# Performance work log

Hardware: AMD Instinct MI355X
Metric: run time of the kernel (lower is better)

The kernel has to match this reference:

```python
import jax, jax.numpy as jnp
import numpy as np

B, N, C, H = 8, 1024, 768, 12
D = C // H          # head_dim = 64
M = 2 * D           # rand_feat_dim = 128
SCALE = D ** -0.5
EPS = 1e-12         # F.normalize eps


def _feature_map(z, rand_matrix):
    # z: [B,H,N,D] already multiplied by sqrt(scale); proj: [H,D,M]
    logits = jnp.einsum('bhnd,hdm->bhnm', z, rand_matrix)
    sqnorm = 0.5 * jnp.sum(z * z, axis=-1, keepdims=True)
    return jnp.exp(logits - sqnorm) * (M ** -0.5)


def setup_inputs() -> dict:
    key = jax.random.key(0)
    k1, k2, k3, k4, k5 = jax.random.split(key, 5)
    x = jax.random.normal(k1, (B, N, C), dtype=jnp.float32)
    qkv_w = jax.random.normal(k2, (3 * C, C), dtype=jnp.float32) * 0.02
    proj_w = jax.random.normal(k3, (C, C), dtype=jnp.float32) * 0.02
    proj_b = jax.random.normal(k4, (C,), dtype=jnp.float32) * 0.02
    rand_matrix = jax.random.normal(k5, (H, D, M), dtype=jnp.float32)
    return {"x": x, "qkv_w": qkv_w, "proj_w": proj_w, "proj_b": proj_b,
            "rand_matrix": rand_matrix}


def reference(x, qkv_w, proj_w, proj_b, rand_matrix):
    b, n, c = x.shape
    # qkv projection (torch Linear, no bias): [B,N,3C] -> [3,B,H,N,D]
    qkv = (x @ qkv_w.T).reshape(b, n, 3, H, D).transpose(2, 0, 3, 1, 4)
    q, k, v = qkv[0], qkv[1], qkv[2]
    sq = SCALE ** 0.5
    qf = _feature_map(q * sq, rand_matrix)   # [B,H,N,M]
    kf = _feature_map(k * sq, rand_matrix)   # [B,H,N,M]
    attn = jnp.einsum('bhnm,bhkm->bhnk', qf, kf)          # explicit O(N^2)
    denom = jnp.maximum(jnp.sum(jnp.abs(attn), axis=-1, keepdims=True), EPS)
    attn = attn / denom                                   # L1 normalize
    out = jnp.einsum('bhnk,bhkd->bhnd', attn, v)          # [B,H,N,D]
    out = out.transpose(0, 2, 1, 3).reshape(b, n, c)
    return out @ proj_w.T + proj_b
```

## Files before the change

kernel.cpp:

```cpp
#include <hip/hip_runtime.h>
#include <hip/hip_bf16.h>

#define PB 8
#define PN 1024
#define PC 768
#define PH 12
#define PD 64
#define PM 128
#define SQ 0.35355339059327373f
#define MSCALE 0.08838834764831843f

typedef _Float16 f16;
typedef f16 f16x8 __attribute__((ext_vector_type(8)));
typedef f16 f16x4 __attribute__((ext_vector_type(4)));
typedef float f32x4 __attribute__((ext_vector_type(4)));

#define GLL(src, dst) __builtin_amdgcn_global_load_lds( \
    (const __attribute__((address_space(1))) void*)(src), \
    (__attribute__((address_space(3))) void*)(dst), 16, 0, 0)

__global__ __launch_bounds__(192) void conv_all(
        const float* __restrict__ x, const float* __restrict__ qkv_w,
        const float* __restrict__ proj_w, const float* __restrict__ rm,
        f16* __restrict__ Ax, f16* __restrict__ Bqk, f16* __restrict__ Bp,
        f16* __restrict__ Rt, float* __restrict__ kvf, float* __restrict__ sf)
{
    const int bid = blockIdx.x;
    const int t = threadIdx.x;
    if (bid < 11264) {
        const float* src; f16* dst; int r;
        if (bid < 8192)       { src = x;      dst = Ax;  r = bid; }
        else if (bid < 10496) { src = qkv_w;  dst = Bqk; r = bid - 8192; }
        else                  { src = proj_w; dst = Bp;  r = bid - 10496; }
        const int c = t * 4;
        float4 v = *(const float4*)&src[(size_t)r * PC + c];
        f16x4 hv;
        hv.x = (f16)v.x; hv.y = (f16)v.y; hv.z = (f16)v.z; hv.w = (f16)v.w;
        *(f16x4*)&dst[(size_t)r * PC + c] = hv;
    } else if (bid < 11276) {
        const int h = bid - 11264;
        for (int e = t; e < PD * PM; e += 192)
            Rt[(size_t)h * 8192 + e] = (f16)rm[(size_t)h * 8192 + (e & 63) * PM + (e >> 6)];
    } else if (bid < 12300) {
        float4 z = make_float4(0.f, 0.f, 0.f, 0.f);
        *(float4*)&kvf[(size_t)(bid - 11276) * 768 + t * 4] = z;
    } else {
        float4 z = make_float4(0.f, 0.f, 0.f, 0.f);
        *(float4*)&sf[(size_t)(bid - 12300) * 768 + t * 4] = z;
    }
}

__global__ __launch_bounds__(256) void gemm_qkv(
        const f16* __restrict__ A,
        const f16* __restrict__ Bm,
        f16* __restrict__ zq, f16* __restrict__ zk, f16* __restrict__ vh,
        float* __restrict__ sqq, float* __restrict__ sqk)
{
    __shared__ f16 As[128 * 64];
    __shared__ f16 Bs[128 * 64];
    const int t = threadIdx.x;
    const int wave = t >> 6, lane = t & 63;
    const int wm = wave >> 1, wn = wave & 1;
    const int bi = blockIdx.x * 128, bj = blockIdx.y * 128;

    f32x4 acc[4][4] = {};

    const int rowi = lane >> 3;
    const int cb = (lane & 7) ^ ((lane >> 4) & 3);
    const f16* ApE = A + (size_t)(bi + wave * 32 + rowi) * PC + cb * 8;
    const f16* ApO = A + (size_t)(bi + wave * 32 + rowi) * PC + (cb ^ 4) * 8;
    const f16* BpE = Bm + (size_t)(bj + wave * 32 + rowi) * PC + cb * 8;
    const f16* BpO = Bm + (size_t)(bj + wave * 32 + rowi) * PC + (cb ^ 4) * 8;
    f16* AsB = &As[wave * 32 * 64];
    f16* BsB = &Bs[wave * 32 * 64];

    const int q4 = lane >> 4;
    for (int kt = 0; kt < 12; ++kt) {
        const int k0 = kt * 64;
        __syncthreads();
        GLL(ApE + k0,               AsB);
        GLL(ApO + k0 + (size_t) 8 * PC, AsB + 8 * 64);
        GLL(ApE + k0 + (size_t)16 * PC, AsB + 16 * 64);
        GLL(ApO + k0 + (size_t)24 * PC, AsB + 24 * 64);
        GLL(BpE + k0,               BsB);
        GLL(BpO + k0 + (size_t) 8 * PC, BsB + 8 * 64);
        GLL(BpE + k0 + (size_t)16 * PC, BsB + 16 * 64);
        GLL(BpO + k0 + (size_t)24 * PC, BsB + 24 * 64);
        __syncthreads();

        #pragma unroll
        for (int kh = 0; kh < 2; ++kh) {
            f16x8 af[4], bf[4];
            #pragma unroll
            for (int i = 0; i < 4; ++i) {
                const int r = wm * 64 + i * 16 + (lane & 15);
                const int p = (kh * 4 + q4) ^ ((r >> 1) & 7);
                af[i] = *(const f16x8*)&As[r * 64 + p * 8];
            }
            #pragma unroll
            for (int j = 0; j < 4; ++j) {
                const int r = wn * 64 + j * 16 + (lane & 15);
                const int p = (kh * 4 + q4) ^ ((r >> 1) & 7);
                bf[j] = *(const f16x8*)&Bs[r * 64 + p * 8];
            }
            #pragma unroll
            for (int i = 0; i < 4; ++i)
                #pragma unroll
                for (int j = 0; j < 4; ++j)
                    acc[i][j] = __builtin_amdgcn_mfma_f32_16x16x32_f16(af[i], bf[j], acc[i][j], 0, 0, 0);
        }
    }

    const int quad = lane >> 4, cc = lane & 15;
    const int colbase = bj + wn * 64;
    const int b = bi >> 10;
    if (colbase < 1536) {
        const int which = colbase >= 768;
        const int h = (colbase - which * 768) >> 6;
        f16* zdst = which ? zk : zq;
        float* sdst = which ? sqk : sqq;
        const size_t bh = (size_t)(b * PH + h);
        #pragma unroll
        for (int i = 0; i < 4; ++i) {
            const int row0 = bi + wm * 64 + i * 16 + quad * 4;
            #pragma unroll
            for (int r = 0; r < 4; ++r) {
                const int n = (row0 + r) & 1023;
                f16 zh[4]; float psq = 0.f;
                #pragma unroll
                for (int j = 0; j < 4; ++j) {
                    zh[j] = (f16)(acc[i][j][r] * SQ);
                    float zf = (float)zh[j];
                    psq += zf * zf;
                }
                psq += __shfl_xor(psq, 1, 64);
                psq += __shfl_xor(psq, 2, 64);
                psq += __shfl_xor(psq, 4, 64);
                psq += __shfl_xor(psq, 8, 64);
                if (cc == 0) sdst[(bh << 10) + n] = 0.5f * psq;
                f16* zp = zdst + (((bh << 10) + n) << 6);
                #pragma unroll
                for (int j = 0; j < 4; ++j) zp[j * 16 + cc] = zh[j];
            }
        }
    } else {
        const int h = (colbase - 1536) >> 6;
        const size_t bh = (size_t)(b * PH + h);
        #pragma unroll
        for (int i = 0; i < 4; ++i) {
            const int row0 = bi + wm * 64 + i * 16 + quad * 4;
            #pragma unroll
            for (int r = 0; r < 4; ++r) {
                const int n = (row0 + r) & 1023;
                f16* vp = vh + (((bh << 10) + n) << 6);
                #pragma unroll
                for (int j = 0; j < 4; ++j) vp[j * 16 + cc] = (f16)acc[i][j][r];
            }
        }
    }
}

__global__ __launch_bounds__(256) void feat_kv(
        const f16* __restrict__ zk, const f16* __restrict__ Rt,
        const float* __restrict__ sqk, const f16* __restrict__ vh,
        float* __restrict__ kvf, float* __restrict__ sf)
{
    __shared__ __align__(16) char smem[52224];
    f16* As = (f16*)smem;
    f16* Bs = (f16*)(smem + 16384);
    f16* Pt = (f16*)smem;
    f16* vT = (f16*)(smem + 34816);
    __shared__ float sqs[128];

    const int t = threadIdx.x;
    const int wave = t >> 6, lane = t & 63;
    const int wm = wave >> 1, wn = wave & 1;
    const int nt = blockIdx.x, bh = blockIdx.y;
    const int h = bh % PH;

    const f16* A = zk + (((size_t)bh << 10) + nt * 128) * 64;
    const f16* Bm = Rt + (size_t)h * (PM * PD);

    if (t < 128) sqs[t] = sqk[((size_t)bh << 10) + nt * 128 + t];

    const int rowi = lane >> 3;
    const int cb = (lane & 7) ^ ((lane >> 4) & 3);
    const f16* ApE = A + (size_t)(wave * 32 + rowi) * 64 + cb * 8;
    const f16* ApO = A + (size_t)(wave * 32 + rowi) * 64 + (cb ^ 4) * 8;
    const f16* BpE = Bm + (size_t)(wave * 32 + rowi) * 64 + cb * 8;
    const f16* BpO = Bm + (size_t)(wave * 32 + rowi) * 64 + (cb ^ 4) * 8;
    f16* AsB = &As[wave * 32 * 64];
    f16* BsB = &Bs[wave * 32 * 64];
    GLL(ApE,            AsB);
    GLL(ApO + 8 * 64,   AsB + 8 * 64);
    GLL(ApE + 16 * 64,  AsB + 16 * 64);
    GLL(ApO + 24 * 64,  AsB + 24 * 64);
    GLL(BpE,            BsB);
    GLL(BpO + 8 * 64,   BsB + 8 * 64);
    GLL(BpE + 16 * 64,  BsB + 16 * 64);
    GLL(BpO + 24 * 64,  BsB + 24 * 64);
    __syncthreads();

    const int q4 = lane >> 4;
    f32x4 acc[4][4] = {};
    #pragma unroll
    for (int kh = 0; kh < 2; ++kh) {
        f16x8 af[4], bf[4];
        #pragma unroll
        for (int i = 0; i < 4; ++i) {
            const int r = wm * 64 + i * 16 + (lane & 15);
            const int p = (kh * 4 + q4) ^ ((r >> 1) & 7);
            af[i] = *(const f16x8*)&As[r * 64 + p * 8];
        }
        #pragma unroll
        for (int j = 0; j < 4; ++j) {
            const int r = wn * 64 + j * 16 + (lane & 15);
            const int p = (kh * 4 + q4) ^ ((r >> 1) & 7);
            bf[j] = *(const f16x8*)&Bs[r * 64 + p * 8];
        }
        #pragma unroll
        for (int i = 0; i < 4; ++i)
            #pragma unroll
            for (int j = 0; j < 4; ++j)
                acc[i][j] = __builtin_amdgcn_mfma_f32_16x16x32_f16(af[i], bf[j], acc[i][j], 0, 0, 0);
    }

    const int quad = lane >> 4, cc = lane & 15;
    __syncthreads();

    #pragma unroll
    for (int i = 0; i < 4; ++i) {
        #pragma unroll
        for (int j = 0; j < 4; ++j) {
            const int col = wn * 64 + j * 16 + cc;
            #pragma unroll
            for (int r = 0; r < 4; ++r) {
                const int rl = wm * 64 + i * 16 + quad * 4 + r;
                Pt[col * 136 + rl] = (f16)(__expf(acc[i][j][r] - sqs[rl]) * MSCALE);
            }
        }
    }
    {
        const int vn = t >> 1;
        const int vhf = (t & 1) * 32;
        const f16* vbase = vh + (((size_t)bh << 10) + nt * 128 + vn) * 64 + vhf;
        #pragma unroll
        for (int k = 0; k < 4; ++k) {
            f16x8 vv = *(const f16x8*)&vbase[k * 8];
            #pragma unroll
            for (int e = 0; e < 8; ++e)
                vT[(vhf + k * 8 + e) * 136 + vn] = vv[e];
        }
    }
    __syncthreads();

    f32x4 acc2[4][2] = {};
    #pragma unroll
    for (int kt = 0; kt < 4; ++kt) {
        const int kb = kt * 32 + (lane >> 4) * 8;
        f16x8 af2[4], bf2[2];
        #pragma unroll
        for (int i = 0; i < 4; ++i)
            af2[i] = *(const f16x8*)&Pt[(wm * 64 + i * 16 + (lane & 15)) * 136 + kb];
        #pragma unroll
        for (int j = 0; j < 2; ++j)
            bf2[j] = *(const f16x8*)&vT[(wn * 32 + j * 16 + (lane & 15)) * 136 + kb];
        #pragma unroll
        for (int i = 0; i < 4; ++i)
            #pragma unroll
            for (int j = 0; j < 2; ++j)
                acc2[i][j] = __builtin_amdgcn_mfma_f32_16x16x32_f16(af2[i], bf2[j], acc2[i][j], 0, 0, 0);
    }

    float* kvo = kvf + (size_t)bh * 8192;
    #pragma unroll
    for (int i = 0; i < 4; ++i) {
        #pragma unroll
        for (int j = 0; j < 2; ++j) {
            const int d = wn * 32 + j * 16 + cc;
            #pragma unroll
            for (int r = 0; r < 4; ++r) {
                const int m = wm * 64 + i * 16 + quad * 4 + r;
                atomicAdd(&kvo[m * 64 + d], acc2[i][j][r]);
            }
        }
    }
    {
        const int sm = t >> 1, shf = (t & 1) * 64;
        float sp = 0.f;
        #pragma unroll
        for (int k = 0; k < 8; ++k) {
            f16x8 pv = *(const f16x8*)&Pt[sm * 136 + shf + k * 8];
            #pragma unroll
            for (int e = 0; e < 8; ++e) sp += (float)pv[e];
        }
        sp += __shfl_xor(sp, 1, 64);
        if ((t & 1) == 0) atomicAdd(&sf[(size_t)bh * 128 + sm], sp);
    }
}

__global__ __launch_bounds__(256) void feat_apply(
        const f16* __restrict__ zq, const f16* __restrict__ Rt,
        const float* __restrict__ sqq, const float* __restrict__ kvf,
        const float* __restrict__ sf, f16* __restrict__ ohA)
{
    __shared__ __align__(16) char smem[52224];
    f16* As = (f16*)smem;
    f16* Bs = (f16*)(smem + 16384);
    f16* Pn = (f16*)smem;
    f16* kvT = (f16*)(smem + 34816);
    __shared__ float sqs[128], ssm[128], dns[128];

    const int t = threadIdx.x;
    const int wave = t >> 6, lane = t & 63;
    const int wm = wave >> 1, wn = wave & 1;
    const int nt = blockIdx.x, bh = blockIdx.y;
    const int b = bh / PH, h = bh % PH;

    const f16* A = zq + (((size_t)bh << 10) + nt * 128) * 64;
    const f16* Bm = Rt + (size_t)h * (PM * PD);

    if (t < 128) {
        sqs[t] = sqq[((size_t)bh << 10) + nt * 128 + t];
        ssm[t] = sf[(size_t)bh * 128 + t];
    }

    const int rowi = lane >> 3;
    const int cb = (lane & 7) ^ ((lane >> 4) & 3);
    const f16* ApE = A + (size_t)(wave * 32 + rowi) * 64 + cb * 8;
    const f16* ApO = A + (size_t)(wave * 32 + rowi) * 64 + (cb ^ 4) * 8;
    const f16* BpE = Bm + (size_t)(wave * 32 + rowi) * 64 + cb * 8;
    const f16* BpO = Bm + (size_t)(wave * 32 + rowi) * 64 + (cb ^ 4) * 8;
    f16* AsB = &As[wave * 32 * 64];
    f16* BsB = &Bs[wave * 32 * 64];
    GLL(ApE,            AsB);
    GLL(ApO + 8 * 64,   AsB + 8 * 64);
    GLL(ApE + 16 * 64,  AsB + 16 * 64);
    GLL(ApO + 24 * 64,  AsB + 24 * 64);
    GLL(BpE,            BsB);
    GLL(BpO + 8 * 64,   BsB + 8 * 64);
    GLL(BpE + 16 * 64,  BsB + 16 * 64);
    GLL(BpO + 24 * 64,  BsB + 24 * 64);
    __syncthreads();

    const int q4 = lane >> 4;
    f32x4 acc[4][4] = {};
    #pragma unroll
    for (int kh = 0; kh < 2; ++kh) {
        f16x8 af[4], bf[4];
        #pragma unroll
        for (int i = 0; i < 4; ++i) {
            const int r = wm * 64 + i * 16 + (lane & 15);
            const int p = (kh * 4 + q4) ^ ((r >> 1) & 7);
            af[i] = *(const f16x8*)&As[r * 64 + p * 8];
        }
        #pragma unroll
        for (int j = 0; j < 4; ++j) {
            const int r = wn * 64 + j * 16 + (lane & 15);
            const int p = (kh * 4 + q4) ^ ((r >> 1) & 7);
            bf[j] = *(const f16x8*)&Bs[r * 64 + p * 8];
        }
        #pragma unroll
        for (int i = 0; i < 4; ++i)
            #pragma unroll
            for (int j = 0; j < 4; ++j)
                acc[i][j] = __builtin_amdgcn_mfma_f32_16x16x32_f16(af[i], bf[j], acc[i][j], 0, 0, 0);
    }

    const int quad = lane >> 4, cc = lane & 15;
    __syncthreads();

    #pragma unroll
    for (int i = 0; i < 4; ++i) {
        #pragma unroll
        for (int j = 0; j < 4; ++j) {
            const int col = wn * 64 + j * 16 + cc;
            #pragma unroll
            for (int r = 0; r < 4; ++r) {
                const int rl = wm * 64 + i * 16 + quad * 4 + r;
                Pn[rl * 136 + col] = (f16)(__expf(acc[i][j][r] - sqs[rl]) * MSCALE);
            }
        }
    }
    {
        const int m = t >> 1;
        const int dh2 = (t & 1) * 32;
        const float* kvb = kvf + ((size_t)bh * 128 + m) * 64 + dh2;
        #pragma unroll
        for (int k = 0; k < 8; ++k) {
            float4 k4 = *(const float4*)&kvb[k * 4];
            kvT[(dh2 + k * 4 + 0) * 136 + m] = (f16)k4.x;
            kvT[(dh2 + k * 4 + 1) * 136 + m] = (f16)k4.y;
            kvT[(dh2 + k * 4 + 2) * 136 + m] = (f16)k4.z;
            kvT[(dh2 + k * 4 + 3) * 136 + m] = (f16)k4.w;
        }
    }
    __syncthreads();

    {
        const int n = t >> 1, mh = (t & 1) * 64;
        float p = 0.f;
        #pragma unroll
        for (int k = 0; k < 8; ++k) {
            f16x8 pv = *(const f16x8*)&Pn[n * 136 + mh + k * 8];
            #pragma unroll
            for (int e = 0; e < 8; ++e)
                p += (float)pv[e] * ssm[mh + k * 8 + e];
        }
        p += __shfl_xor(p, 1, 64);
        if ((t & 1) == 0) dns[n] = (p < 1e-12f) ? 1e-12f : p;
    }
    __syncthreads();

    f32x4 acc3[4][2] = {};
    #pragma unroll
    for (int kt = 0; kt < 4; ++kt) {
        const int kb = kt * 32 + (lane >> 4) * 8;
        f16x8 af3[4], bf3[2];
        #pragma unroll
        for (int i = 0; i < 4; ++i)
            af3[i] = *(const f16x8*)&Pn[(wm * 64 + i * 16 + (lane & 15)) * 136 + kb];
        #pragma unroll
        for (int j = 0; j < 2; ++j)
            bf3[j] = *(const f16x8*)&kvT[(wn * 32 + j * 16 + (lane & 15)) * 136 + kb];
        #pragma unroll
        for (int i = 0; i < 4; ++i)
            #pragma unroll
            for (int j = 0; j < 2; ++j)
                acc3[i][j] = __builtin_amdgcn_mfma_f32_16x16x32_f16(af3[i], bf3[j], acc3[i][j], 0, 0, 0);
    }

    f16* ob = ohA + ((size_t)(b * PN) + nt * 128) * PC + h * PD;
    #pragma unroll
    for (int i = 0; i < 4; ++i) {
        #pragma unroll
        for (int j = 0; j < 2; ++j) {
            const int d = wn * 32 + j * 16 + cc;
            #pragma unroll
            for (int r = 0; r < 4; ++r) {
                const int n = wm * 64 + i * 16 + quad * 4 + r;
                ob[(size_t)n * PC + d] = (f16)(acc3[i][j][r] / dns[n]);
            }
        }
    }
}

__global__ __launch_bounds__(256) void gemm_proj(
        const f16* __restrict__ A,
        const f16* __restrict__ Bm,
        float* __restrict__ Cm, const float* __restrict__ bias)
{
    __shared__ f16 As[128 * 64];
    __shared__ f16 Bs[64 * 64];
    const int t = threadIdx.x;
    const int wave = t >> 6, lane = t & 63;
    const int wm = wave >> 1, wn = wave & 1;
    const int bi = blockIdx.x * 128, bj = blockIdx.y * 64;

    f32x4 acc[4][2] = {};

    const int rowi = lane >> 3;
    const int cb = (lane & 7) ^ ((lane >> 4) & 3);
    const f16* ApE = A + (size_t)(bi + wave * 32 + rowi) * PC + cb * 8;
    const f16* ApO = A + (size_t)(bi + wave * 32 + rowi) * PC + (cb ^ 4) * 8;
    const f16* BpE = Bm + (size_t)(bj + wave * 16 + rowi) * PC + cb * 8;
    const f16* BpO = Bm + (size_t)(bj + wave * 16 + rowi) * PC + (cb ^ 4) * 8;
    f16* AsB = &As[wave * 32 * 64];
    f16* BsB = &Bs[wave * 16 * 64];

    const int q4 = lane >> 4;
    for (int kt = 0; kt < 12; ++kt) {
        const int k0 = kt * 64;
        __syncthreads();
        GLL(ApE + k0,               AsB);
        GLL(ApO + k0 + (size_t) 8 * PC, AsB + 8 * 64);
        GLL(ApE + k0 + (size_t)16 * PC, AsB + 16 * 64);
        GLL(ApO + k0 + (size_t)24 * PC, AsB + 24 * 64);
        GLL(BpE + k0,               BsB);
        GLL(BpO + k0 + (size_t) 8 * PC, BsB + 8 * 64);
        __syncthreads();

        #pragma unroll
        for (int kh = 0; kh < 2; ++kh) {
            f16x8 af[4], bf[2];
            #pragma unroll
            for (int i = 0; i < 4; ++i) {
                const int r = wm * 64 + i * 16 + (lane & 15);
                const int p = (kh * 4 + q4) ^ ((r >> 1) & 7);
                af[i] = *(const f16x8*)&As[r * 64 + p * 8];
            }
            #pragma unroll
            for (int j = 0; j < 2; ++j) {
                const int r = wn * 32 + j * 16 + (lane & 15);
                const int p = (kh * 4 + q4) ^ ((r >> 1) & 7);
                bf[j] = *(const f16x8*)&Bs[r * 64 + p * 8];
            }
            #pragma unroll
            for (int i = 0; i < 4; ++i)
                #pragma unroll
                for (int j = 0; j < 2; ++j)
                    acc[i][j] = __builtin_amdgcn_mfma_f32_16x16x32_f16(af[i], bf[j], acc[i][j], 0, 0, 0);
        }
    }

    const int cr = (lane >> 4) * 4, cc = lane & 15;
    #pragma unroll
    for (int i = 0; i < 4; ++i) {
        const int row = bi + wm * 64 + i * 16 + cr;
        #pragma unroll
        for (int j = 0; j < 2; ++j) {
            const int col = bj + wn * 32 + j * 16 + cc;
            const float bv = bias[col];
            #pragma unroll
            for (int r = 0; r < 4; ++r)
                Cm[(size_t)(row + r) * PC + col] = acc[i][j][r] + bv;
        }
    }
}

extern "C" void kernel_launch(void* const* d_in, const int* in_sizes, int n_in,
                              void* d_out, int out_size, void* d_ws, size_t ws_size,
                              hipStream_t stream) {
    const float* x      = (const float*)d_in[0];
    const float* qkv_w  = (const float*)d_in[1];
    const float* proj_w = (const float*)d_in[2];
    const float* proj_b = (const float*)d_in[3];
    const float* rm     = (const float*)d_in[4];
    float* out = (float*)d_out;

    char* ws = (char*)d_ws;
    f16*   Ax   = (f16*)(ws);
    f16*   Bqk  = (f16*)(ws + 12582912);
    f16*   Bp   = (f16*)(ws + 16121856);
    f16*   Rt   = (f16*)(ws + 17301504);
    f16*   zq   = (f16*)(ws + 17498112);
    f16*   zk   = (f16*)(ws + 30081024);
    f16*   vh   = (f16*)(ws + 42663936);
    float* sqq  = (float*)(ws + 55246848);
    float* sqk  = (float*)(ws + 55640064);
    float* kvf  = (float*)(ws + 56033280);
    float* sf   = (float*)(ws + 59179008);
    f16*   ohA  = (f16*)(ws + 59228160);

    conv_all<<<12316, 192, 0, stream>>>(x, qkv_w, proj_w, rm, Ax, Bqk, Bp, Rt, kvf, sf);

    gemm_qkv<<<dim3(64, 18), 256, 0, stream>>>(Ax, Bqk, zq, zk, vh, sqq, sqk);

    feat_kv<<<dim3(8, 96), 256, 0, stream>>>(zk, Rt, sqk, vh, kvf, sf);

    feat_apply<<<dim3(8, 96), 256, 0, stream>>>(zq, Rt, sqq, kvf, sf, ohA);

    gemm_proj<<<dim3(64, 12), 256, 0, stream>>>(ohA, Bp, out, proj_b);
}
```

Baseline: 191.1 us.

## Double-buffer GEMM LDS tiles and replace KV atomics with partial-sum reduction

Both GEMM kernels now stage the next K tile into a second LDS buffer while computing on the current one, hiding global-load latency at the cost of doubled shared memory. feat_kv writes per-tile partial KV and feature sums to workspace buffers instead of using atomicAdd, and a new kv_reduce kernel sums them. This also removes the zero-init blocks from the conversion kernel. V and KV loads are hoisted earlier to overlap with the first GEMM stage, and the partial buffers reuse dead workspace regions.

```diff
diff --git a/kernel.cpp b/kernel.cpp
--- a/kernel.cpp
+++ b/kernel.cpp
@@ -23,7 +23,7 @@
         const float* __restrict__ x, const float* __restrict__ qkv_w,
         const float* __restrict__ proj_w, const float* __restrict__ rm,
         f16* __restrict__ Ax, f16* __restrict__ Bqk, f16* __restrict__ Bp,
-        f16* __restrict__ Rt, float* __restrict__ kvf, float* __restrict__ sf)
+        f16* __restrict__ Rt)
 {
     const int bid = blockIdx.x;
     const int t = threadIdx.x;
@@ -37,16 +37,10 @@
         f16x4 hv;
         hv.x = (f16)v.x; hv.y = (f16)v.y; hv.z = (f16)v.z; hv.w = (f16)v.w;
         *(f16x4*)&dst[(size_t)r * PC + c] = hv;
-    } else if (bid < 11276) {
+    } else {
         const int h = bid - 11264;
         for (int e = t; e < PD * PM; e += 192)
             Rt[(size_t)h * 8192 + e] = (f16)rm[(size_t)h * 8192 + (e & 63) * PM + (e >> 6)];
-    } else if (bid < 12300) {
-        float4 z = make_float4(0.f, 0.f, 0.f, 0.f);
-        *(float4*)&kvf[(size_t)(bid - 11276) * 768 + t * 4] = z;
-    } else {
-        float4 z = make_float4(0.f, 0.f, 0.f, 0.f);
-        *(float4*)&sf[(size_t)(bid - 12300) * 768 + t * 4] = z;
     }
 }
 
@@ -56,8 +50,8 @@
         f16* __restrict__ zq, f16* __restrict__ zk, f16* __restrict__ vh,
         float* __restrict__ sqq, float* __restrict__ sqk)
 {
-    __shared__ f16 As[128 * 64];
-    __shared__ f16 Bs[128 * 64];
+    __shared__ f16 As[2][8192];
+    __shared__ f16 Bs[2][8192];
     const int t = threadIdx.x;
     const int wave = t >> 6, lane = t & 63;
     const int wm = wave >> 1, wn = wave & 1;
@@ -71,22 +65,24 @@
     const f16* ApO = A + (size_t)(bi + wave * 32 + rowi) * PC + (cb ^ 4) * 8;
     const f16* BpE = Bm + (size_t)(bj + wave * 32 + rowi) * PC + cb * 8;
     const f16* BpO = Bm + (size_t)(bj + wave * 32 + rowi) * PC + (cb ^ 4) * 8;
-    f16* AsB = &As[wave * 32 * 64];
-    f16* BsB = &Bs[wave * 32 * 64];
+
+#define STG(BUF, KT) do { const int k0_ = (KT) * 64; \
+    GLL(ApE + k0_,                   &As[BUF][wave * 2048]); \
+    GLL(ApO + k0_ + (size_t) 8 * PC, &As[BUF][wave * 2048 +  512]); \
+    GLL(ApE + k0_ + (size_t)16 * PC, &As[BUF][wave * 2048 + 1024]); \
+    GLL(ApO + k0_ + (size_t)24 * PC, &As[BUF][wave * 2048 + 1536]); \
+    GLL(BpE + k0_,                   &Bs[BUF][wave * 2048]); \
+    GLL(BpO + k0_ + (size_t) 8 * PC, &Bs[BUF][wave * 2048 +  512]); \
+    GLL(BpE + k0_ + (size_t)16 * PC, &Bs[BUF][wave * 2048 + 1024]); \
+    GLL(BpO + k0_ + (size_t)24 * PC, &Bs[BUF][wave * 2048 + 1536]); } while(0)
 
     const int q4 = lane >> 4;
+    STG(0, 0);
+    __syncthreads();
+
     for (int kt = 0; kt < 12; ++kt) {
-        const int k0 = kt * 64;
-        __syncthreads();
-        GLL(ApE + k0,               AsB);
-        GLL(ApO + k0 + (size_t) 8 * PC, AsB + 8 * 64);
-        GLL(ApE + k0 + (size_t)16 * PC, AsB + 16 * 64);
-        GLL(ApO + k0 + (size_t)24 * PC, AsB + 24 * 64);
-        GLL(BpE + k0,               BsB);
-        GLL(BpO + k0 + (size_t) 8 * PC, BsB + 8 * 64);
-        GLL(BpE + k0 + (size_t)16 * PC, BsB + 16 * 64);
-        GLL(BpO + k0 + (size_t)24 * PC, BsB + 24 * 64);
-        __syncthreads();
+        const int cur = kt & 1;
+        if (kt < 11) STG(cur ^ 1, kt + 1);
 
         #pragma unroll
         for (int kh = 0; kh < 2; ++kh) {
@@ -95,13 +91,13 @@
             for (int i = 0; i < 4; ++i) {
                 const int r = wm * 64 + i * 16 + (lane & 15);
                 const int p = (kh * 4 + q4) ^ ((r >> 1) & 7);
-                af[i] = *(const f16x8*)&As[r * 64 + p * 8];
+                af[i] = *(const f16x8*)&As[cur][r * 64 + p * 8];
             }
             #pragma unroll
             for (int j = 0; j < 4; ++j) {
                 const int r = wn * 64 + j * 16 + (lane & 15);
                 const int p = (kh * 4 + q4) ^ ((r >> 1) & 7);
-                bf[j] = *(const f16x8*)&Bs[r * 64 + p * 8];
+                bf[j] = *(const f16x8*)&Bs[cur][r * 64 + p * 8];
             }
             #pragma unroll
             for (int i = 0; i < 4; ++i)
@@ -109,7 +105,9 @@
                 for (int j = 0; j < 4; ++j)
                     acc[i][j] = __builtin_amdgcn_mfma_f32_16x16x32_f16(af[i], bf[j], acc[i][j], 0, 0, 0);
         }
-    }
+        __syncthreads();
+    }
+#undef STG
 
     const int quad = lane >> 4, cc = lane & 15;
     const int colbase = bj + wn * 64;
@@ -163,7 +161,7 @@
 __global__ __launch_bounds__(256) void feat_kv(
         const f16* __restrict__ zk, const f16* __restrict__ Rt,
         const float* __restrict__ sqk, const f16* __restrict__ vh,
-        float* __restrict__ kvf, float* __restrict__ sf)
+        float* __restrict__ kvpA, float* __restrict__ kvpB, float* __restrict__ sfp)
 {
     __shared__ __align__(16) char smem[52224];
     f16* As = (f16*)smem;
@@ -182,6 +180,14 @@
     const f16* Bm = Rt + (size_t)h * (PM * PD);
 
     if (t < 128) sqs[t] = sqk[((size_t)bh << 10) + nt * 128 + t];
+
+    const int vn = t >> 1;
+    const int vhf = (t & 1) * 32;
+    const f16* vbase = vh + (((size_t)bh << 10) + nt * 128 + vn) * 64 + vhf;
+    f16x8 vpre0 = *(const f16x8*)&vbase[0];
+    f16x8 vpre1 = *(const f16x8*)&vbase[8];
+    f16x8 vpre2 = *(const f16x8*)&vbase[16];
+    f16x8 vpre3 = *(const f16x8*)&vbase[24];
 
     const int rowi = lane >> 3;
     const int cb = (lane & 7) ^ ((lane >> 4) & 3);
@@ -241,15 +247,12 @@
         }
     }
     {
-        const int vn = t >> 1;
-        const int vhf = (t & 1) * 32;
-        const f16* vbase = vh + (((size_t)bh << 10) + nt * 128 + vn) * 64 + vhf;
-        #pragma unroll
-        for (int k = 0; k < 4; ++k) {
-            f16x8 vv = *(const f16x8*)&vbase[k * 8];
-            #pragma unroll
-            for (int e = 0; e < 8; ++e)
-                vT[(vhf + k * 8 + e) * 136 + vn] = vv[e];
+        #pragma unroll
+        for (int e = 0; e < 8; ++e) {
+            vT[(vhf +      e) * 136 + vn] = vpre0[e];
+            vT[(vhf +  8 + e) * 136 + vn] = vpre1[e];
+            vT[(vhf + 16 + e) * 136 + vn] = vpre2[e];
+            vT[(vhf + 24 + e) * 136 + vn] = vpre3[e];
         }
     }
     __syncthreads();
@@ -272,7 +275,8 @@
                 acc2[i][j] = __builtin_amdgcn_mfma_f32_16x16x32_f16(af2[i], bf2[j], acc2[i][j], 0, 0, 0);
     }
 
-    float* kvo = kvf + (size_t)bh * 8192;
+    float* kvo = ((nt < 4) ? (kvpA + (size_t)nt * 786432)
+                           : (kvpB + (size_t)(nt - 4) * 786432)) + (size_t)bh * 8192;
     #pragma unroll
     for (int i = 0; i < 4; ++i) {
         #pragma unroll
@@ -281,7 +285,7 @@
             #pragma unroll
             for (int r = 0; r < 4; ++r) {
                 const int m = wm * 64 + i * 16 + quad * 4 + r;
-                atomicAdd(&kvo[m * 64 + d], acc2[i][j][r]);
+                kvo[m * 64 + d] = acc2[i][j][r];
             }
         }
     }
@@ -295,8 +299,39 @@
             for (int e = 0; e < 8; ++e) sp += (float)pv[e];
         }
         sp += __shfl_xor(sp, 1, 64);
-        if ((t & 1) == 0) atomicAdd(&sf[(size_t)bh * 128 + sm], sp);
-    }
+        if ((t & 1) == 0) sfp[((size_t)nt * 96 + bh) * 128 + sm] = sp;
+    }
+}
+
+__global__ __launch_bounds__(256) void kv_reduce(
+        const float* __restrict__ kvpA, const float* __restrict__ kvpB,
+        const float* __restrict__ sfp, float* __restrict__ kvf, float* __restrict__ sf)
+{
+    const int bh = blockIdx.x;
+    if (blockIdx.y == 8) {
+        const int t = threadIdx.x;
+        if (t < 128) {
+            float s = 0.f;
+            #pragma unroll
+            for (int nt = 0; nt < 8; ++nt)
+                s += sfp[((size_t)nt * 96 + bh) * 128 + t];
+            sf[(size_t)bh * 128 + t] = s;
+        }
+        return;
+    }
+    const size_t base = (size_t)bh * 8192 + blockIdx.y * 1024 + threadIdx.x * 4;
+    float4 s = *(const float4*)&kvpA[base];
+    #pragma unroll
+    for (int nt = 1; nt < 4; ++nt) {
+        float4 v = *(const float4*)&kvpA[(size_t)nt * 786432 + base];
+        s.x += v.x; s.y += v.y; s.z += v.z; s.w += v.w;
+    }
+    #pragma unroll
+    for (int nt = 0; nt < 4; ++nt) {
+        float4 v = *(const float4*)&kvpB[(size_t)nt * 786432 + base];
+        s.x += v.x; s.y += v.y; s.z += v.z; s.w += v.w;
+    }
+    *(float4*)&kvf[base] = s;
 }
 
 __global__ __launch_bounds__(256) void feat_apply(
@@ -324,6 +359,13 @@
         sqs[t] = sqq[((size_t)bh << 10) + nt * 128 + t];
         ssm[t] = sf[(size_t)bh * 128 + t];
     }
+
+    const int m_ = t >> 1;
+    const int dh2 = (t & 1) * 32;
+    const float* kvb = kvf + ((size_t)bh * 128 + m_) * 64 + dh2;
+    float4 kpre[8];
+    #pragma unroll
+    for (int k = 0; k < 8; ++k) kpre[k] = *(const float4*)&kvb[k * 4];
 
     const int rowi = lane >> 3;
     const int cb = (lane & 7) ^ ((lane >> 4) & 3);
@@ -383,16 +425,12 @@
         }
     }
     {
-        const int m = t >> 1;
-        const int dh2 = (t & 1) * 32;
-        const float* kvb = kvf + ((size_t)bh * 128 + m) * 64 + dh2;
         #pragma unroll
         for (int k = 0; k < 8; ++k) {
-            float4 k4 = *(const float4*)&kvb[k * 4];
-            kvT[(dh2 + k * 4 + 0) * 136 + m] = (f16)k4.x;
-            kvT[(dh2 + k * 4 + 1) * 136 + m] = (f16)k4.y;
-            kvT[(dh2 + k * 4 + 2) * 136 + m] = (f16)k4.z;
-            kvT[(dh2 + k * 4 + 3) * 136 + m] = (f16)k4.w;
+            kvT[(dh2 + k * 4 + 0) * 136 + m_] = (f16)kpre[k].x;
+            kvT[(dh2 + k * 4 + 1) * 136 + m_] = (f16)kpre[k].y;
+            kvT[(dh2 + k * 4 + 2) * 136 + m_] = (f16)kpre[k].z;
+            kvT[(dh2 + k * 4 + 3) * 136 + m_] = (f16)kpre[k].w;
         }
     }
     __syncthreads();
@@ -450,8 +488,8 @@
         const f16* __restrict__ Bm,
         float* __restrict__ Cm, const float* __restrict__ bias)
 {
-    __shared__ f16 As[128 * 64];
-    __shared__ f16 Bs[64 * 64];
+    __shared__ f16 As[2][8192];
+    __shared__ f16 Bs[2][4096];
     const int t = threadIdx.x;
     const int wave = t >> 6, lane = t & 63;
     const int wm = wave >> 1, wn = wave & 1;
@@ -465,20 +503,22 @@
     const f16* ApO = A + (size_t)(bi + wave * 32 + rowi) * PC + (cb ^ 4) * 8;
     const f16* BpE = Bm + (size_t)(bj + wave * 16 + rowi) * PC + cb * 8;
     const f16* BpO = Bm + (size_t)(bj + wave * 16 + rowi) * PC + (cb ^ 4) * 8;
-    f16* AsB = &As[wave * 32 * 64];
-    f16* BsB = &Bs[wave * 16 * 64];
+
+#define STGP(BUF, KT) do { const int k0_ = (KT) * 64; \
+    GLL(ApE + k0_,                   &As[BUF][wave * 2048]); \
+    GLL(ApO + k0_ + (size_t) 8 * PC, &As[BUF][wave * 2048 +  512]); \
+    GLL(ApE + k0_ + (size_t)16 * PC, &As[BUF][wave * 2048 + 1024]); \
+    GLL(ApO + k0_ + (size_t)24 * PC, &As[BUF][wave * 2048 + 1536]); \
+    GLL(BpE + k0_,                   &Bs[BUF][wave * 1024]); \
+    GLL(BpO + k0_ + (size_t) 8 * PC, &Bs[BUF][wave * 1024 + 512]); } while(0)
 
     const int q4 = lane >> 4;
+    STGP(0, 0);
+    __syncthreads();
+
     for (int kt = 0; kt < 12; ++kt) {
-        const int k0 = kt * 64;
-        __syncthreads();
-        GLL(ApE + k0,               AsB);
-        GLL(ApO + k0 + (size_t) 8 * PC, AsB + 8 * 64);
-        GLL(ApE + k0 + (size_t)16 * PC, AsB + 16 * 64);
-        GLL(ApO + k0 + (size_t)24 * PC, AsB + 24 * 64);
-        GLL(BpE + k0,               BsB);
-        GLL(BpO + k0 + (size_t) 8 * PC, BsB + 8 * 64);
-        __syncthreads();
+        const int cur = kt & 1;
+        if (kt < 11) STGP(cur ^ 1, kt + 1);
 
         #pragma unroll
         for (int kh = 0; kh < 2; ++kh) {
@@ -487,13 +527,13 @@
             for (int i = 0; i < 4; ++i) {
                 const int r = wm * 64 + i * 16 + (lane & 15);
                 const int p = (kh * 4 + q4) ^ ((r >> 1) & 7);
-                af[i] = *(const f16x8*)&As[r * 64 + p * 8];
+                af[i] = *(const f16x8*)&As[cur][r * 64 + p * 8];
             }
             #pragma unroll
             for (int j = 0; j < 2; ++j) {
                 const int r = wn * 32 + j * 16 + (lane & 15);
                 const int p = (kh * 4 + q4) ^ ((r >> 1) & 7);
-                bf[j] = *(const f16x8*)&Bs[r * 64 + p * 8];
+                bf[j] = *(const f16x8*)&Bs[cur][r * 64 + p * 8];
             }
             #pragma unroll
             for (int i = 0; i < 4; ++i)
@@ -501,7 +541,9 @@
                 for (int j = 0; j < 2; ++j)
                     acc[i][j] = __builtin_amdgcn_mfma_f32_16x16x32_f16(af[i], bf[j], acc[i][j], 0, 0, 0);
         }
-    }
+        __syncthreads();
+    }
+#undef STGP
 
     const int cr = (lane >> 4) * 4, cc = lane & 15;
     #pragma unroll
@@ -542,11 +584,17 @@
     float* sf   = (float*)(ws + 59179008);
     f16*   ohA  = (f16*)(ws + 59228160);
 
-    conv_all<<<12316, 192, 0, stream>>>(x, qkv_w, proj_w, rm, Ax, Bqk, Bp, Rt, kvf, sf);
+    float* kvpA = (float*)(ws);
+    float* kvpB = (float*)(ws + 59228160);
+    float* sfp  = (float*)(ws + 12582912);
+
+    conv_all<<<11276, 192, 0, stream>>>(x, qkv_w, proj_w, rm, Ax, Bqk, Bp, Rt);
 
     gemm_qkv<<<dim3(64, 18), 256, 0, stream>>>(Ax, Bqk, zq, zk, vh, sqq, sqk);
 
-    feat_kv<<<dim3(8, 96), 256, 0, stream>>>(zk, Rt, sqk, vh, kvf, sf);
+    feat_kv<<<dim3(8, 96), 256, 0, stream>>>(zk, Rt, sqk, vh, kvpA, kvpB, sfp);
+
+    kv_reduce<<<dim3(96, 9), 256, 0, stream>>>(kvpA, kvpB, sfp, kvf, sf);
 
     feat_apply<<<dim3(8, 96), 256, 0, stream>>>(zq, Rt, sqq, kvf, sf, ohA);
 
```

Result: no change. 193.0 us (+1.0%).

## Stage QKV epilogue through LDS and replace KV atomics with partial-sum reduction

Applied to the files above, without the earlier changes.

The QKV GEMM epilogue now writes each wave's 64x64 tile into swizzled shared memory. It then stores it to zq/zk/vh as coalesced 16-byte row segments, instead of scattered 2-byte stores. feat_kv no longer does float atomicAdd into kvf and sf. It writes per-tile partial results into scratch buffers that alias dead workspace regions, and a new kv_reduce kernel sums the eight partials. This removes the atomic traffic and the zero-initialisation blocks in conv_all, at the cost of an extra kernel launch and roughly 25 MB of extra partial-buffer reads and writes.

```diff
diff --git a/kernel.cpp b/kernel.cpp
--- a/kernel.cpp
+++ b/kernel.cpp
@@ -23,7 +23,7 @@
         const float* __restrict__ x, const float* __restrict__ qkv_w,
         const float* __restrict__ proj_w, const float* __restrict__ rm,
         f16* __restrict__ Ax, f16* __restrict__ Bqk, f16* __restrict__ Bp,
-        f16* __restrict__ Rt, float* __restrict__ kvf, float* __restrict__ sf)
+        f16* __restrict__ Rt)
 {
     const int bid = blockIdx.x;
     const int t = threadIdx.x;
@@ -37,16 +37,10 @@
         f16x4 hv;
         hv.x = (f16)v.x; hv.y = (f16)v.y; hv.z = (f16)v.z; hv.w = (f16)v.w;
         *(f16x4*)&dst[(size_t)r * PC + c] = hv;
-    } else if (bid < 11276) {
+    } else {
         const int h = bid - 11264;
         for (int e = t; e < PD * PM; e += 192)
             Rt[(size_t)h * 8192 + e] = (f16)rm[(size_t)h * 8192 + (e & 63) * PM + (e >> 6)];
-    } else if (bid < 12300) {
-        float4 z = make_float4(0.f, 0.f, 0.f, 0.f);
-        *(float4*)&kvf[(size_t)(bid - 11276) * 768 + t * 4] = z;
-    } else {
-        float4 z = make_float4(0.f, 0.f, 0.f, 0.f);
-        *(float4*)&sf[(size_t)(bid - 12300) * 768 + t * 4] = z;
     }
 }
 
@@ -111,9 +105,14 @@
         }
     }
 
+    __syncthreads();
+    f16* W = (wave < 2 ? As : Bs) + (wave & 1) * 4096;
     const int quad = lane >> 4, cc = lane & 15;
+    const int rr = lane >> 3, c8 = lane & 7;
     const int colbase = bj + wn * 64;
     const int b = bi >> 10;
+    const int nb = (bi & 1023) + wm * 64;
+
     if (colbase < 1536) {
         const int which = colbase >= 768;
         const int h = (colbase - which * 768) >> 6;
@@ -122,10 +121,9 @@
         const size_t bh = (size_t)(b * PH + h);
         #pragma unroll
         for (int i = 0; i < 4; ++i) {
-            const int row0 = bi + wm * 64 + i * 16 + quad * 4;
             #pragma unroll
             for (int r = 0; r < 4; ++r) {
-                const int n = (row0 + r) & 1023;
+                const int li = i * 16 + quad * 4 + r;
                 f16 zh[4]; float psq = 0.f;
                 #pragma unroll
                 for (int j = 0; j < 4; ++j) {
@@ -137,25 +135,40 @@
                 psq += __shfl_xor(psq, 2, 64);
                 psq += __shfl_xor(psq, 4, 64);
                 psq += __shfl_xor(psq, 8, 64);
-                if (cc == 0) sdst[(bh << 10) + n] = 0.5f * psq;
-                f16* zp = zdst + (((bh << 10) + n) << 6);
+                if (cc == 0) sdst[(bh << 10) + nb + li] = 0.5f * psq;
                 #pragma unroll
-                for (int j = 0; j < 4; ++j) zp[j * 16 + cc] = zh[j];
-            }
+                for (int j = 0; j < 4; ++j)
+                    W[li * 64 + ((j * 16 + cc) ^ (quad << 4))] = zh[j];
+            }
+        }
+        asm volatile("" ::: "memory");
+        #pragma unroll
+        for (int it = 0; it < 8; ++it) {
+            const int row = it * 8 + rr;
+            const int s = ((row >> 2) & 3) << 4;
+            f16x8 vv = *(const f16x8*)&W[row * 64 + ((c8 * 8) ^ s)];
+            *(f16x8*)&zdst[(((bh << 10) + nb + row) << 6) + c8 * 8] = vv;
         }
     } else {
         const int h = (colbase - 1536) >> 6;
         const size_t bh = (size_t)(b * PH + h);
         #pragma unroll
         for (int i = 0; i < 4; ++i) {
-            const int row0 = bi + wm * 64 + i * 16 + quad * 4;
             #pragma unroll
             for (int r = 0; r < 4; ++r) {
-                const int n = (row0 + r) & 1023;
-                f16* vp = vh + (((bh << 10) + n) << 6);
+                const int li = i * 16 + quad * 4 + r;
                 #pragma unroll
-                for (int j = 0; j < 4; ++j) vp[j * 16 + cc] = (f16)acc[i][j][r];
-            }
+                for (int j = 0; j < 4; ++j)
+                    W[li * 64 + ((j * 16 + cc) ^ (quad << 4))] = (f16)acc[i][j][r];
+            }
+        }
+        asm volatile("" ::: "memory");
+        #pragma unroll
+        for (int it = 0; it < 8; ++it) {
+            const int row = it * 8 + rr;
+            const int s = ((row >> 2) & 3) << 4;
+            f16x8 vv = *(const f16x8*)&W[row * 64 + ((c8 * 8) ^ s)];
+            *(f16x8*)&vh[(((bh << 10) + nb + row) << 6) + c8 * 8] = vv;
         }
     }
 }
@@ -163,7 +176,7 @@
 __global__ __launch_bounds__(256) void feat_kv(
         const f16* __restrict__ zk, const f16* __restrict__ Rt,
         const float* __restrict__ sqk, const f16* __restrict__ vh,
-        float* __restrict__ kvf, float* __restrict__ sf)
+        float* __restrict__ kvpA, float* __restrict__ kvpB, float* __restrict__ sfp)
 {
     __shared__ __align__(16) char smem[52224];
     f16* As = (f16*)smem;
@@ -272,7 +285,8 @@
                 acc2[i][j] = __builtin_amdgcn_mfma_f32_16x16x32_f16(af2[i], bf2[j], acc2[i][j], 0, 0, 0);
     }
 
-    float* kvo = kvf + (size_t)bh * 8192;
+    float* kvo = ((nt < 4) ? (kvpA + (size_t)nt * 786432)
+                           : (kvpB + (size_t)(nt - 4) * 786432)) + (size_t)bh * 8192;
     #pragma unroll
     for (int i = 0; i < 4; ++i) {
         #pragma unroll
@@ -281,7 +295,7 @@
             #pragma unroll
             for (int r = 0; r < 4; ++r) {
                 const int m = wm * 64 + i * 16 + quad * 4 + r;
-                atomicAdd(&kvo[m * 64 + d], acc2[i][j][r]);
+                kvo[m * 64 + d] = acc2[i][j][r];
             }
         }
     }
@@ -295,8 +309,39 @@
             for (int e = 0; e < 8; ++e) sp += (float)pv[e];
         }
         sp += __shfl_xor(sp, 1, 64);
-        if ((t & 1) == 0) atomicAdd(&sf[(size_t)bh * 128 + sm], sp);
-    }
+        if ((t & 1) == 0) sfp[((size_t)nt * 96 + bh) * 128 + sm] = sp;
+    }
+}
+
+__global__ __launch_bounds__(256) void kv_reduce(
+        const float* __restrict__ kvpA, const float* __restrict__ kvpB,
+        const float* __restrict__ sfp, float* __restrict__ kvf, float* __restrict__ sf)
+{
+    const int bh = blockIdx.x;
+    if (blockIdx.y == 8) {
+        const int t = threadIdx.x;
+        if (t < 128) {
+            float s = 0.f;
+            #pragma unroll
+            for (int nt = 0; nt < 8; ++nt)
+                s += sfp[((size_t)nt * 96 + bh) * 128 + t];
+            sf[(size_t)bh * 128 + t] = s;
+        }
+        return;
+    }
+    const size_t base = (size_t)bh * 8192 + blockIdx.y * 1024 + threadIdx.x * 4;
+    float4 s = *(const float4*)&kvpA[base];
+    #pragma unroll
+    for (int nt = 1; nt < 4; ++nt) {
+        float4 v = *(const float4*)&kvpA[(size_t)nt * 786432 + base];
+        s.x += v.x; s.y += v.y; s.z += v.z; s.w += v.w;
+    }
+    #pragma unroll
+    for (int nt = 0; nt < 4; ++nt) {
+        float4 v = *(const float4*)&kvpB[(size_t)nt * 786432 + base];
+        s.x += v.x; s.y += v.y; s.z += v.z; s.w += v.w;
+    }
+    *(float4*)&kvf[base] = s;
 }
 
 __global__ __launch_bounds__(256) void feat_apply(
@@ -542,11 +587,17 @@
     float* sf   = (float*)(ws + 59179008);
     f16*   ohA  = (f16*)(ws + 59228160);
 
-    conv_all<<<12316, 192, 0, stream>>>(x, qkv_w, proj_w, rm, Ax, Bqk, Bp, Rt, kvf, sf);
+    float* kvpA = (float*)(ws);
+    float* kvpB = (float*)(ws + 59228160);
+    float* sfp  = (float*)(ws + 12582912);
+
+    conv_all<<<11276, 192, 0, stream>>>(x, qkv_w, proj_w, rm, Ax, Bqk, Bp, Rt);
 
     gemm_qkv<<<dim3(64, 18), 256, 0, stream>>>(Ax, Bqk, zq, zk, vh, sqq, sqk);
 
-    feat_kv<<<dim3(8, 96), 256, 0, stream>>>(zk, Rt, sqk, vh, kvf, sf);
+    feat_kv<<<dim3(8, 96), 256, 0, stream>>>(zk, Rt, sqk, vh, kvpA, kvpB, sfp);
+
+    kv_reduce<<<dim3(96, 9), 256, 0, stream>>>(kvpA, kvpB, sfp, kvf, sf);
 
     feat_apply<<<dim3(8, 96), 256, 0, stream>>>(zq, Rt, sqq, kvf, sf, ohA);
 
```

Result: faster. 180.9 us (-5.4%).
